# Kernel tuning notes

Measured on AMD Instinct MI355X. Metric: run time of the kernel, lower is better.

The kernel has to match this reference:

```python
import jax, jax.numpy as jnp
import numpy as np

NEG = -9e15

def setup_inputs() -> dict:
    key = jax.random.key(0)
    k1, k2, k3, k4, k5 = jax.random.split(key, 5)
    N, Fin, Fout = 8192, 256, 128
    h = jax.random.normal(k1, (N, Fin), dtype=jnp.float32)
    adj = jax.random.randint(k2, (N, N), 0, 2, dtype=jnp.int32)
    # Parameters (xavier_uniform with gain=1.414 for a1/a2; kaiming-like for W is fine as random init)
    lim_w = float(np.sqrt(6.0 / (Fin + Fout)))
    W = jax.random.uniform(k3, (Fout, Fin), dtype=jnp.float32, minval=-lim_w, maxval=lim_w)
    lim_a = float(1.414 * np.sqrt(6.0 / (Fout + 1)))
    a1 = jax.random.uniform(k4, (Fout, 1), dtype=jnp.float32, minval=-lim_a, maxval=lim_a)
    a2 = jax.random.uniform(k5, (Fout, 1), dtype=jnp.float32, minval=-lim_a, maxval=lim_a)
    return {"h": h, "adj": adj, "W": W, "a1": a1, "a2": a2}

def reference(h, adj, W, a1, a2):
    Wh = h @ W.T                                   # [N, Fout]
    s1 = (Wh @ a1)                                 # [N, 1]
    s2 = (Wh @ a2)                                 # [N, 1]
    e = jax.nn.leaky_relu(s1 + s2.T, 0.2)          # [N, N]
    att = jnp.where(adj > 0, e, jnp.float32(NEG))
    att = jax.nn.softmax(att, axis=1)
    h_prime = att @ Wh                             # [N, Fout]
    return jax.nn.elu(h_prime)
```

## Files before the change

kernel.cpp:

```cpp
#include <hip/hip_runtime.h>
#include <cstdint>
#include <cstddef>

#define N_NODES 8192
#define FIN 256
#define FOUT 128
#define MT 32
#define KC 256
#define JS 4
#define JW (N_NODES / JS)
#define NCHS (JW / KC)
#define LOG2E 1.4426950408889634f

typedef __attribute__((ext_vector_type(8))) short bf16x8;
typedef __attribute__((ext_vector_type(4))) float f32x4;
typedef __attribute__((ext_vector_type(4))) int i32x4;
typedef __attribute__((ext_vector_type(4))) unsigned int u32x4;

__device__ __forceinline__ float bf2f(unsigned short u) {
    union { unsigned int i; float f; } v; v.i = ((unsigned int)u) << 16; return v.f;
}
__device__ __forceinline__ unsigned short f2bf(float f) {
    union { float f; unsigned int i; } v; v.f = f;
    unsigned int r = (v.i + 0x7FFFu + ((v.i >> 16) & 1u)) >> 16;
    return (unsigned short)r;
}
__device__ __forceinline__ unsigned int pack_bf16(float a, float b) {
    return (unsigned)f2bf(a) | ((unsigned)f2bf(b) << 16);
}

__device__ __forceinline__ size_t whb_idx(int j, int f) {
    return ((size_t)((j >> 5) * 8 + (f >> 4)) << 9) + (((j >> 3) & 3) << 7)
         + ((f & 15) << 3) + (j & 7);
}

__global__ __launch_bounds__(256) void wh_kernel(const float* __restrict__ h,
                                                 const float* __restrict__ W,
                                                 unsigned short* __restrict__ whB) {
    __shared__ float hT[64][FIN + 5];
    const int t = threadIdx.x;
    const int i0 = blockIdx.x * 64;
    const int f0 = blockIdx.y * 32;
#pragma unroll
    for (int c = 0; c < 16; ++c) {
        int chunk = c * 256 + t;
        int row = chunk >> 6, col = (chunk & 63) * 4;
        f32x4 v = *(const f32x4*)&h[(size_t)(i0 + row) * FIN + col];
        hT[row][col] = v[0]; hT[row][col + 1] = v[1];
        hT[row][col + 2] = v[2]; hT[row][col + 3] = v[3];
    }
    __syncthreads();
    const int lane = t & 63;
    const int fb8 = __builtin_amdgcn_readfirstlane(f0 + (t >> 6) * 8);
    const float* w0 = W + (size_t)fb8 * FIN;
    float acc[8] = {0.f, 0.f, 0.f, 0.f, 0.f, 0.f, 0.f, 0.f};
    for (int k = 0; k < FIN; k += 4) {
        float h0 = hT[lane][k],     h1 = hT[lane][k + 1];
        float h2 = hT[lane][k + 2], h3 = hT[lane][k + 3];
#pragma unroll
        for (int c = 0; c < 8; ++c) {
            const float* wr = w0 + c * FIN;
            acc[c] += h0 * wr[k] + h1 * wr[k + 1] + h2 * wr[k + 2] + h3 * wr[k + 3];
        }
    }
    const int i = i0 + lane;
#pragma unroll
    for (int c = 0; c < 8; ++c)
        whB[whb_idx(i, fb8 + c)] = f2bf(acc[c]);
}

__global__ __launch_bounds__(256) void s_kernel(const unsigned short* __restrict__ whB,
                                                const float* __restrict__ a1,
                                                const float* __restrict__ a2,
                                                float* __restrict__ s1,
                                                float* __restrict__ s2) {
    __shared__ float p1[4][64], p2[4][64];
    const int t = threadIdx.x;
    const int l = t & 63;
    const int g = t >> 6;
    const int i = blockIdx.x * 64 + l;
    float acc1 = 0.f, acc2 = 0.f;
#pragma unroll
    for (int fb = g * 2; fb < g * 2 + 2; ++fb) {
#pragma unroll
        for (int sl = 0; sl < 16; ++sl) {
            int f = fb * 16 + sl;
            float v = bf2f(whB[whb_idx(i, f)]);
            acc1 += v * a1[f];
            acc2 += v * a2[f];
        }
    }
    p1[g][l] = acc1; p2[g][l] = acc2;
    __syncthreads();
    if (g == 0) {
        s1[i] = (p1[0][l] + p1[1][l] + p1[2][l] + p1[3][l]) * LOG2E;
        s2[i] = (p2[0][l] + p2[1][l] + p2[2][l] + p2[3][l]) * LOG2E;
    }
}

__global__ __launch_bounds__(256) void gat_kernel(const int* __restrict__ adj,
                                                  const unsigned short* __restrict__ whB,
                                                  const float* __restrict__ s1,
                                                  const float* __restrict__ s2,
                                                  float* __restrict__ out,
                                                  float* __restrict__ nums,
                                                  float* __restrict__ dens) {
    __shared__ __align__(16) unsigned short sP[MT][KC + 8];
    __shared__ float sDen[MT];
    __shared__ float sS1[MT];
    const int t = threadIdx.x;
    const int slice = blockIdx.x & (JS - 1);
    const int i0 = (blockIdx.x >> 2) * MT;
    const int jb = slice * JW;
    const int kb0 = slice * (JW / 32);
    float* __restrict__ num = slice ? (nums + (size_t)(slice - 1) * N_NODES * FOUT) : out;
    float* __restrict__ den = dens + (size_t)slice * N_NODES;
    if (t < MT) { sDen[t] = 0.f; sS1[t] = s1[i0 + t]; }
    __syncthreads();

    const int r0 = t >> 4;
    const int s  = t & 15;
    const int lane = t & 63;
    const int quad = lane >> 4;
    const int sl = lane & 15;
    const int wv = t >> 6;
    const int* __restrict__ aRow0 = adj + (size_t)(i0 + r0) * N_NODES + jb;
    const int* __restrict__ aRow1 = aRow0 + (size_t)16 * N_NODES;
    const float s1a = sS1[r0];
    const float s1b = sS1[r0 + 16];

    f32x4 acc00 = {0.f,0.f,0.f,0.f}, acc01 = {0.f,0.f,0.f,0.f};
    f32x4 acc10 = {0.f,0.f,0.f,0.f}, acc11 = {0.f,0.f,0.f,0.f};

    for (int ch = 0; ch < NCHS; ++ch) {
        const int cb = ch * KC + s * 16;
        i32x4 av0[4], av1[4];
        f32x4 sv[4];
#pragma unroll
        for (int q = 0; q < 4; ++q) {
            av0[q] = *(const i32x4*)&aRow0[cb + q * 4];
            av1[q] = *(const i32x4*)&aRow1[cb + q * 4];
            sv[q]  = *(const f32x4*)&s2[jb + cb + q * 4];
        }
        float part0 = 0.f, part1 = 0.f;
        unsigned int w0[8], w1[8];
#pragma unroll
        for (int q = 0; q < 4; ++q) {
            float p0[4], p1v[4];
#pragma unroll
            for (int r = 0; r < 4; ++r) {
                float y0 = s1a + sv[q][r];
                float y1 = s1b + sv[q][r];
                y0 = fmaxf(y0, 0.2f * y0);
                y1 = fmaxf(y1, 0.2f * y1);
                float e0 = __builtin_amdgcn_exp2f(y0);
                float e1 = __builtin_amdgcn_exp2f(y1);
                p0[r]  = (av0[q][r] > 0) ? e0 : 0.f;
                p1v[r] = (av1[q][r] > 0) ? e1 : 0.f;
                part0 += p0[r];
                part1 += p1v[r];
            }
            w0[2 * q]     = pack_bf16(p0[0], p0[1]);
            w0[2 * q + 1] = pack_bf16(p0[2], p0[3]);
            w1[2 * q]     = pack_bf16(p1v[0], p1v[1]);
            w1[2 * q + 1] = pack_bf16(p1v[2], p1v[3]);
        }
        u32x4 ra = {w0[0], w0[1], w0[2], w0[3]};
        u32x4 rb = {w0[4], w0[5], w0[6], w0[7]};
        u32x4 rc = {w1[0], w1[1], w1[2], w1[3]};
        u32x4 rd = {w1[4], w1[5], w1[6], w1[7]};
        *(u32x4*)&sP[r0][s * 16]          = ra;
        *(u32x4*)&sP[r0][s * 16 + 8]      = rb;
        *(u32x4*)&sP[r0 + 16][s * 16]     = rc;
        *(u32x4*)&sP[r0 + 16][s * 16 + 8] = rd;
        part0 += __shfl_xor(part0, 1); part1 += __shfl_xor(part1, 1);
        part0 += __shfl_xor(part0, 2); part1 += __shfl_xor(part1, 2);
        part0 += __shfl_xor(part0, 4); part1 += __shfl_xor(part1, 4);
        part0 += __shfl_xor(part0, 8); part1 += __shfl_xor(part1, 8);
        if (s == 0) { sDen[r0] += part0; sDen[r0 + 16] += part1; }
        __syncthreads();
#pragma unroll
        for (int kq = 0; kq < KC / 32; ++kq) {
            bf16x8 a0  = *(const bf16x8*)&sP[sl][kq * 32 + quad * 8];
            bf16x8 a1f = *(const bf16x8*)&sP[16 + sl][kq * 32 + quad * 8];
            int kb = kb0 + ch * (KC / 32) + kq;
            const unsigned short* t0 = whB + ((size_t)(kb * 8 + wv * 2) << 9) + lane * 8;
            bf16x8 b0 = *(const bf16x8*)t0;
            bf16x8 b1 = *(const bf16x8*)(t0 + 512);
            acc00 = __builtin_amdgcn_mfma_f32_16x16x32_bf16(a0,  b0, acc00, 0, 0, 0);
            acc01 = __builtin_amdgcn_mfma_f32_16x16x32_bf16(a0,  b1, acc01, 0, 0, 0);
            acc10 = __builtin_amdgcn_mfma_f32_16x16x32_bf16(a1f, b0, acc10, 0, 0, 0);
            acc11 = __builtin_amdgcn_mfma_f32_16x16x32_bf16(a1f, b1, acc11, 0, 0, 0);
        }
        __syncthreads();
    }
    if (t < MT) den[i0 + t] = sDen[t];
#pragma unroll
    for (int m = 0; m < 2; ++m) {
#pragma unroll
        for (int nn = 0; nn < 2; ++nn) {
            f32x4 a = (m == 0) ? (nn == 0 ? acc00 : acc01) : (nn == 0 ? acc10 : acc11);
#pragma unroll
            for (int r = 0; r < 4; ++r) {
                int row = m * 16 + quad * 4 + r;
                num[(size_t)(i0 + row) * FOUT + wv * 32 + nn * 16 + sl] = a[r];
            }
        }
    }
}

__global__ __launch_bounds__(256) void fin_kernel(float* __restrict__ out,
                                                  const float* __restrict__ nums,
                                                  const float* __restrict__ dens) {
    const int idx = blockIdx.x * 256 + threadIdx.x;
    const int i = idx >> 7;
    const size_t NF = (size_t)N_NODES * FOUT;
    float numv = out[idx] + nums[idx] + nums[NF + idx] + nums[2 * NF + idx];
    float denv = dens[i] + dens[N_NODES + i] + dens[2 * N_NODES + i] + dens[3 * N_NODES + i];
    float v = numv / fmaxf(denv, 1e-30f);
    out[idx] = (v > 0.f) ? v : expm1f(v);
}

extern "C" void kernel_launch(void* const* d_in, const int* in_sizes, int n_in,
                              void* d_out, int out_size, void* d_ws, size_t ws_size,
                              hipStream_t stream) {
    const float* h   = (const float*)d_in[0];
    const int*   adj = (const int*)d_in[1];
    const float* W   = (const float*)d_in[2];
    const float* a1  = (const float*)d_in[3];
    const float* a2  = (const float*)d_in[4];

    char* ws = (char*)d_ws;
    unsigned short* whB = (unsigned short*)ws;
    float* s1   = (float*)(ws + (4u << 20));
    float* s2   = s1 + N_NODES;
    float* dens = s2 + N_NODES;
    float* nums = dens + 4 * N_NODES;
    float* out  = (float*)d_out;

    wh_kernel<<<dim3(N_NODES / 64, FOUT / 32), 256, 0, stream>>>(h, W, whB);
    s_kernel<<<dim3(N_NODES / 64), 256, 0, stream>>>(whB, a1, a2, s1, s2);
    gat_kernel<<<dim3((N_NODES / MT) * JS), 256, 0, stream>>>(adj, whB, s1, s2,
                                                              out, nums, dens);
    fin_kernel<<<dim3(N_NODES * FOUT / 256), 256, 0, stream>>>(out, nums, dens);
}
```

Measured before the change: 406.7 us.

## Remap adjacency loads per wave, prefetch next chunk, defer denominator reduction

```diff
diff --git a/kernel.cpp b/kernel.cpp
--- a/kernel.cpp
+++ b/kernel.cpp
@@ -15,7 +15,7 @@
 typedef __attribute__((ext_vector_type(8))) short bf16x8;
 typedef __attribute__((ext_vector_type(4))) float f32x4;
 typedef __attribute__((ext_vector_type(4))) int i32x4;
-typedef __attribute__((ext_vector_type(4))) unsigned int u32x4;
+typedef __attribute__((ext_vector_type(2))) unsigned int u32x2;
 
 __device__ __forceinline__ float bf2f(unsigned short u) {
     union { unsigned int i; float f; } v; v.i = ((unsigned int)u) << 16; return v.f;
@@ -98,7 +98,7 @@
     }
 }
 
-__global__ __launch_bounds__(256) void gat_kernel(const int* __restrict__ adj,
+__global__ __launch_bounds__(256, 4) void gat_kernel(const int* __restrict__ adj,
                                                   const unsigned short* __restrict__ whB,
                                                   const float* __restrict__ s1,
                                                   const float* __restrict__ s2,
@@ -106,8 +106,6 @@
                                                   float* __restrict__ nums,
                                                   float* __restrict__ dens) {
     __shared__ __align__(16) unsigned short sP[MT][KC + 8];
-    __shared__ float sDen[MT];
-    __shared__ float sS1[MT];
     const int t = threadIdx.x;
     const int slice = blockIdx.x & (JS - 1);
     const int i0 = (blockIdx.x >> 2) * MT;
@@ -115,69 +113,51 @@
     const int kb0 = slice * (JW / 32);
     float* __restrict__ num = slice ? (nums + (size_t)(slice - 1) * N_NODES * FOUT) : out;
     float* __restrict__ den = dens + (size_t)slice * N_NODES;
-    if (t < MT) { sDen[t] = 0.f; sS1[t] = s1[i0 + t]; }
-    __syncthreads();
-
-    const int r0 = t >> 4;
-    const int s  = t & 15;
+
     const int lane = t & 63;
+    const int wv = t >> 6;
     const int quad = lane >> 4;
     const int sl = lane & 15;
-    const int wv = t >> 6;
-    const int* __restrict__ aRow0 = adj + (size_t)(i0 + r0) * N_NODES + jb;
-    const int* __restrict__ aRow1 = aRow0 + (size_t)16 * N_NODES;
-    const float s1a = sS1[r0];
-    const float s1b = sS1[r0 + 16];
+
+    float s1r[8];
+#pragma unroll
+    for (int e = 0; e < 8; ++e) s1r[e] = s1[i0 + wv * 8 + e];
+
+    const int* __restrict__ aBase = adj + (size_t)(i0 + wv * 8) * N_NODES + jb + lane * 4;
 
     f32x4 acc00 = {0.f,0.f,0.f,0.f}, acc01 = {0.f,0.f,0.f,0.f};
     f32x4 acc10 = {0.f,0.f,0.f,0.f}, acc11 = {0.f,0.f,0.f,0.f};
+    float denAcc[8] = {0.f,0.f,0.f,0.f,0.f,0.f,0.f,0.f};
+
+    i32x4 av[8];
+    f32x4 sv;
+#pragma unroll
+    for (int e = 0; e < 8; ++e) av[e] = *(const i32x4*)(aBase + (size_t)e * N_NODES);
+    sv = *(const f32x4*)&s2[jb + lane * 4];
 
     for (int ch = 0; ch < NCHS; ++ch) {
-        const int cb = ch * KC + s * 16;
-        i32x4 av0[4], av1[4];
-        f32x4 sv[4];
-#pragma unroll
-        for (int q = 0; q < 4; ++q) {
-            av0[q] = *(const i32x4*)&aRow0[cb + q * 4];
-            av1[q] = *(const i32x4*)&aRow1[cb + q * 4];
-            sv[q]  = *(const f32x4*)&s2[jb + cb + q * 4];
-        }
-        float part0 = 0.f, part1 = 0.f;
-        unsigned int w0[8], w1[8];
-#pragma unroll
-        for (int q = 0; q < 4; ++q) {
-            float p0[4], p1v[4];
+#pragma unroll
+        for (int e = 0; e < 8; ++e) {
+            float p[4];
 #pragma unroll
             for (int r = 0; r < 4; ++r) {
-                float y0 = s1a + sv[q][r];
-                float y1 = s1b + sv[q][r];
-                y0 = fmaxf(y0, 0.2f * y0);
-                y1 = fmaxf(y1, 0.2f * y1);
-                float e0 = __builtin_amdgcn_exp2f(y0);
-                float e1 = __builtin_amdgcn_exp2f(y1);
-                p0[r]  = (av0[q][r] > 0) ? e0 : 0.f;
-                p1v[r] = (av1[q][r] > 0) ? e1 : 0.f;
-                part0 += p0[r];
-                part1 += p1v[r];
+                float y = s1r[e] + sv[r];
+                y = fmaxf(y, 0.2f * y);
+                float ev = __builtin_amdgcn_exp2f(y);
+                p[r] = (av[e][r] > 0) ? ev : 0.f;
+                denAcc[e] += p[r];
             }
-            w0[2 * q]     = pack_bf16(p0[0], p0[1]);
-            w0[2 * q + 1] = pack_bf16(p0[2], p0[3]);
-            w1[2 * q]     = pack_bf16(p1v[0], p1v[1]);
-            w1[2 * q + 1] = pack_bf16(p1v[2], p1v[3]);
-        }
-        u32x4 ra = {w0[0], w0[1], w0[2], w0[3]};
-        u32x4 rb = {w0[4], w0[5], w0[6], w0[7]};
-        u32x4 rc = {w1[0], w1[1], w1[2], w1[3]};
-        u32x4 rd = {w1[4], w1[5], w1[6], w1[7]};
-        *(u32x4*)&sP[r0][s * 16]          = ra;
-        *(u32x4*)&sP[r0][s * 16 + 8]      = rb;
-        *(u32x4*)&sP[r0 + 16][s * 16]     = rc;
-        *(u32x4*)&sP[r0 + 16][s * 16 + 8] = rd;
-        part0 += __shfl_xor(part0, 1); part1 += __shfl_xor(part1, 1);
-        part0 += __shfl_xor(part0, 2); part1 += __shfl_xor(part1, 2);
-        part0 += __shfl_xor(part0, 4); part1 += __shfl_xor(part1, 4);
-        part0 += __shfl_xor(part0, 8); part1 += __shfl_xor(part1, 8);
-        if (s == 0) { sDen[r0] += part0; sDen[r0 + 16] += part1; }
+            u32x2 pk;
+            pk.x = pack_bf16(p[0], p[1]);
+            pk.y = pack_bf16(p[2], p[3]);
+            *(u32x2*)&sP[wv * 8 + e][lane * 4] = pk;
+        }
+        if (ch + 1 < NCHS) {
+            const int* an = aBase + (ch + 1) * KC;
+#pragma unroll
+            for (int e = 0; e < 8; ++e) av[e] = *(const i32x4*)(an + (size_t)e * N_NODES);
+            sv = *(const f32x4*)&s2[jb + (ch + 1) * KC + lane * 4];
+        }
         __syncthreads();
 #pragma unroll
         for (int kq = 0; kq < KC / 32; ++kq) {
@@ -194,7 +174,13 @@
         }
         __syncthreads();
     }
-    if (t < MT) den[i0 + t] = sDen[t];
+#pragma unroll
+    for (int e = 0; e < 8; ++e) {
+        float v = denAcc[e];
+        v += __shfl_xor(v, 1);  v += __shfl_xor(v, 2);  v += __shfl_xor(v, 4);
+        v += __shfl_xor(v, 8);  v += __shfl_xor(v, 16); v += __shfl_xor(v, 32);
+        if (lane == 0) den[i0 + wv * 8 + e] = v;
+    }
 #pragma unroll
     for (int m = 0; m < 2; ++m) {
 #pragma unroll
```

After: 417.8 us. +2.7%, slower.
